# Kernel optimization log

Measured on AMD Instinct MI355X. Metric: run time of the kernel, lower is better.

## Reference

```python
import jax, jax.numpy as jnp
import numpy as np

PRUNING_THRESHOLD = 0.02


def setup_inputs() -> dict:
    key = jax.random.key(0)
    ks = jax.random.split(key, 9)
    B, T, D = 2, 2048, 512
    H, S = 8, 16
    hd = D // H
    x = jax.random.normal(ks[0], (B, T, D), dtype=jnp.float32)
    Wqkv = jax.random.normal(ks[1], (3 * D, D), dtype=jnp.float32) * 0.02
    Wout = jax.random.normal(ks[2], (D, D), dtype=jnp.float32) * 0.02
    splat_centers = jax.random.normal(ks[3], (H, S, hd), dtype=jnp.float32) * 0.3
    splat_deltas = jax.random.normal(ks[4], (H, S, hd), dtype=jnp.float32) * 0.05
    splat_log_scales = jax.random.normal(ks[5], (H, S), dtype=jnp.float32) * 0.2 + jnp.float32(np.log(0.5))
    splat_log_amplitudes = jax.random.normal(ks[6], (H, S), dtype=jnp.float32) * 0.1 - 0.5
    movement_scale = jnp.float32(0.08)
    temperature = jnp.float32(1.0)
    return {"x": x, "Wqkv": Wqkv, "Wout": Wout,
            "splat_centers": splat_centers, "splat_deltas": splat_deltas,
            "splat_log_scales": splat_log_scales, "splat_log_amplitudes": splat_log_amplitudes,
            "movement_scale": movement_scale, "temperature": temperature}


def reference(x, Wqkv, Wout, splat_centers, splat_deltas,
              splat_log_scales, splat_log_amplitudes, movement_scale, temperature):
    B, T, D = x.shape
    H, S, hd = splat_centers.shape
    # qkv projection (nn.Linear: y = x @ W.T), split into q,k,v per head
    qkv = (x @ Wqkv.T).reshape(B, T, 3, H, hd)
    q, k, v = qkv[:, :, 0], qkv[:, :, 1], qkv[:, :, 2]  # [B,T,H,hd]
    # effective centers with bounded movement (eval mode: no warmup)
    bounded_scale = jax.nn.sigmoid(movement_scale) * 0.2
    centers = splat_centers + splat_deltas * bounded_scale  # [H,S,hd]
    scales = jnp.clip(jnp.exp(splat_log_scales), 0.01, 2.0)  # [H,S]
    amplitudes = jnp.clip(jnp.exp(splat_log_amplitudes), 1e-06, 10.0)
    amplitudes = amplitudes * (amplitudes > PRUNING_THRESHOLD).astype(amplitudes.dtype)
    # squared distances from tokens to splat centers: [B,T,H,S]
    q_dists = jnp.sum((q[:, :, :, None, :] - centers[None, None]) ** 2, axis=-1)
    k_dists = jnp.sum((k[:, :, :, None, :] - centers[None, None]) ** 2, axis=-1)
    inv_var = 1.0 / (scales ** 2 + 1e-08)  # [H,S]
    q_w = jnp.exp(-0.5 * q_dists * inv_var)  # [B,T,H,S]
    k_w = jnp.exp(-0.5 * k_dists * inv_var)
    # per-head splat-weighted logits: [B,T(query i),T(key j),H]
    logits = jnp.einsum('bihs,bjhs,hs->bijh', q_w, k_w, amplitudes)
    temp = jnp.clip(temperature, 0.1, 10.0)
    # NOTE: original vectorized path softmaxes over dim=1 (query axis) -- faithful
    attn = jax.nn.softmax(logits / temp, axis=1)
    out = jnp.einsum('btjh,bjhd->bthd', attn, v).reshape(B, T, D)
    return out @ Wout.T
```

## Files before the change

kernel.cpp:

```cpp
#include <hip/hip_runtime.h>
#include <hip/hip_bf16.h>
#include <hip/hip_fp16.h>
#include <cstdint>
#include <cstddef>

#define T_SEQ 2048
#define NBATCH 2
#define DIMD 512
#define NH 8
#define NS 16
#define HD 64
#define NBH 16

using s16x8 = __attribute__((ext_vector_type(8))) short;
using f32x4 = __attribute__((ext_vector_type(4))) float;

static __device__ inline unsigned short f2bf(float f) {
  __hip_bfloat16 h = __float2bfloat16(f);
  return reinterpret_cast<unsigned short&>(h);
}
static __device__ inline unsigned short f2h(float f) {
  __half h = __float2half(f);
  return reinterpret_cast<unsigned short&>(h);
}
static __device__ inline float h2f(unsigned short u) {
  __half h = reinterpret_cast<__half&>(u);
  return __half2float(h);
}
static __device__ inline unsigned int pack2(float a, float b) {
  return (unsigned int)f2bf(a) | ((unsigned int)f2bf(b) << 16);
}
static __device__ inline void gload16(const void* g, void* l) {
  __builtin_amdgcn_global_load_lds((const __attribute__((address_space(1))) void*)g,
                                   (__attribute__((address_space(3))) void*)l, 16, 0, 0);
}
static __device__ inline int swz_id() {
  int nwg = gridDim.x * gridDim.y;
  int orig = blockIdx.y * gridDim.x + blockIdx.x;
  return (orig & 7) * (nwg >> 3) + (orig >> 3);
}

static const size_t OFF_VBUF = 0;
static const size_t OFF_AOUT = 2097152;
static const size_t OFF_XH   = 6291456;
static const size_t OFF_WQH  = 8388608;
static const size_t OFF_WOH  = 9175040;
static const size_t OFF_QABF = 9437184;
static const size_t OFF_KWBF = 9961472;
static const size_t OFF_SPART= 10485760;
static const size_t OFF_VPART= 10616832;
static const size_t OFF_CADJ = 10633216;
static const size_t OFF_IVAR = 10641408;
static const size_t OFF_AMPT = 10641536;

__global__ __launch_bounds__(256) void prep(
    const float* __restrict__ x, const float* __restrict__ Wqkv, const float* __restrict__ Wout,
    const float* __restrict__ centers, const float* __restrict__ deltas,
    const float* __restrict__ lsc, const float* __restrict__ lam,
    const float* __restrict__ ms, const float* __restrict__ tp,
    unsigned short* __restrict__ xh, unsigned short* __restrict__ wqh,
    unsigned short* __restrict__ woh,
    float* __restrict__ cadj, float* __restrict__ ivar, float* __restrict__ ampt) {
  int bid = blockIdx.x;
  int tid = threadIdx.x;
  if (bid == 3072) {
    float bscale = 0.2f / (1.0f + expf(-ms[0]));
    float tclip = fminf(fmaxf(tp[0], 0.1f), 10.0f);
    if (tid < NH * NS) {
      float sc = fminf(fmaxf(expf(lsc[tid]), 0.01f), 2.0f);
      ivar[tid] = 1.0f / (sc * sc + 1e-8f);
      float am = fminf(fmaxf(expf(lam[tid]), 1e-6f), 10.0f);
      am = (am > 0.02f) ? am : 0.0f;
      ampt[tid] = am / tclip;
    }
    for (int e = tid; e < NH * NS * HD; e += 256)
      cadj[e] = centers[e] + deltas[e] * bscale;
    return;
  }
  const float* src; unsigned short* dh; int i4;
  if (bid < 2048)      { src = x;    dh = xh;  i4 = bid * 256 + tid; }
  else if (bid < 2816) { src = Wqkv; dh = wqh; i4 = (bid - 2048) * 256 + tid; }
  else                 { src = Wout; dh = woh; i4 = (bid - 2816) * 256 + tid; }
  float4 v = *(const float4*)&src[(size_t)i4 * 4];
  ushort4 hh;
  hh.x = f2h(v.x); hh.y = f2h(v.y); hh.z = f2h(v.z); hh.w = f2h(v.w);
  *(ushort4*)&dh[(size_t)i4 * 4] = hh;
}

template<int BM, int BN>
__device__ __forceinline__ void gemm_core(
    const unsigned short* Ah, const unsigned short* Bh,
    int K, int m0, int n0,
    unsigned short* ash, unsigned short* bsh,
    f32x4 (&acc)[BM / 32][BN / 32]) {
  constexpr int WM = BM / 2, WN = BN / 2;
  constexpr int MF = WM / 16, NF = WN / 16;
  constexpr int NSA = BM / 8, NSB = BN / 8;
  constexpr int TSEG = NSA + NSB;
  int tid = threadIdx.x;
  int w = tid >> 6, l = tid & 63, lm = l & 15, lq = l >> 4;
  int wm = w >> 1, wn = w & 1;
  int r8 = l >> 3, c8 = l & 7;
  int ksl = (c8 ^ (r8 & 7)) << 3;
#pragma unroll
  for (int mi = 0; mi < MF; ++mi)
#pragma unroll
    for (int ni = 0; ni < NF; ++ni) acc[mi][ni] = (f32x4){0.f, 0.f, 0.f, 0.f};

  for (int k0 = 0; k0 < K; k0 += 64) {
    __syncthreads();
#pragma unroll
    for (int t = 0; t < TSEG / 4; ++t) {
      int s = w + t * 4;
      if (s < NSA) {
        gload16(&Ah[(size_t)(m0 + s * 8 + r8) * K + k0 + ksl], &ash[s * 512]);
      } else {
        int ss = s - NSA;
        gload16(&Bh[(size_t)(n0 + ss * 8 + r8) * K + k0 + ksl], &bsh[ss * 512]);
      }
    }
    __syncthreads();
#pragma unroll
    for (int kh = 0; kh < 2; ++kh) {
      s16x8 fah[MF], fbh[NF];
#pragma unroll
      for (int mi = 0; mi < MF; ++mi) {
        int rr = wm * WM + mi * 16 + lm;
        int off = rr * 64 + ((((kh << 2) | lq) ^ (rr & 7)) << 3);
        fah[mi] = *(const s16x8*)&ash[off];
      }
#pragma unroll
      for (int ni = 0; ni < NF; ++ni) {
        int cc = wn * WN + ni * 16 + lm;
        int off = cc * 64 + ((((kh << 2) | lq) ^ (cc & 7)) << 3);
        fbh[ni] = *(const s16x8*)&bsh[off];
      }
#pragma unroll
      for (int mi = 0; mi < MF; ++mi)
#pragma unroll
        for (int ni = 0; ni < NF; ++ni)
          acc[mi][ni] = __builtin_amdgcn_mfma_f32_16x16x32_f16(fah[mi], fbh[ni], acc[mi][ni], 0, 0, 0);
    }
  }
}

template<int BM, int BN>
__device__ __forceinline__ void write_c(
    float* C, int ldc, int m0, int n0, f32x4 (&acc)[BM / 32][BN / 32]) {
  constexpr int WM = BM / 2, WN = BN / 2;
  int tid = threadIdx.x;
  int w = tid >> 6, l = tid & 63, lm = l & 15, lq = l >> 4;
  int wm = w >> 1, wn = w & 1;
#pragma unroll
  for (int mi = 0; mi < BM / 32; ++mi)
#pragma unroll
    for (int ni = 0; ni < BN / 32; ++ni)
#pragma unroll
      for (int r = 0; r < 4; ++r) {
        int row = m0 + wm * WM + mi * 16 + lq * 4 + r;
        int col = n0 + wn * WN + ni * 16 + lm;
        C[(size_t)row * ldc + col] = acc[mi][ni][r];
      }
}

template<int BM, int BN>
__device__ __forceinline__ void write_ch(
    unsigned short* C, int ldc, int m0, int n0, f32x4 (&acc)[BM / 32][BN / 32]) {
  constexpr int WM = BM / 2, WN = BN / 2;
  int tid = threadIdx.x;
  int w = tid >> 6, l = tid & 63, lm = l & 15, lq = l >> 4;
  int wm = w >> 1, wn = w & 1;
#pragma unroll
  for (int mi = 0; mi < BM / 32; ++mi)
#pragma unroll
    for (int ni = 0; ni < BN / 32; ++ni)
#pragma unroll
      for (int r = 0; r < 4; ++r) {
        int row = m0 + wm * WM + mi * 16 + lq * 4 + r;
        int col = n0 + wn * WN + ni * 16 + lm;
        C[(size_t)row * ldc + col] = f2h(acc[mi][ni][r]);
      }
}

__global__ __launch_bounds__(256) void gemm_qkv(
    const unsigned short* __restrict__ xh, const unsigned short* __restrict__ wqh,
    const float* __restrict__ cadj, const float* __restrict__ ivar,
    const float* __restrict__ ampt, unsigned short* __restrict__ vbuf,
    unsigned short* __restrict__ qa_bf, unsigned short* __restrict__ kw_bf) {
  __shared__ __align__(16) char smem[39168];
  unsigned short* ash = (unsigned short*)smem;
  unsigned short* bsh = (unsigned short*)(smem + 16384);
  int sid = swz_id();
  int bx = sid % 24, by = sid / 24;
  int m0 = by * 128;
  int tid = threadIdx.x;
  f32x4 acc[4][2];
  if (bx >= 16) {
    gemm_core<128, 64>(xh, wqh + (size_t)(1024 + (bx - 16) * 64) * 512,
                       512, m0, 0, ash, bsh, acc);
    write_ch<128, 64>(vbuf, 512, m0, (bx - 16) * 64, acc);
    return;
  }
  bool isk = bx >= 8;
  int h = bx & 7;
  gemm_core<128, 64>(xh, wqh + (size_t)((isk ? 512 : 0) + h * 64) * 512,
                     512, m0, 0, ash, bsh, acc);
  __syncthreads();
  float* q_s = (float*)smem;
  float* c_s = (float*)(smem + 34816);
  {
    int w = tid >> 6, l = tid & 63, lm = l & 15, lq = l >> 4;
    int wm = w >> 1, wn = w & 1;
#pragma unroll
    for (int mi = 0; mi < 4; ++mi)
#pragma unroll
      for (int ni = 0; ni < 2; ++ni)
#pragma unroll
        for (int r = 0; r < 4; ++r)
          q_s[(wm * 64 + mi * 16 + lq * 4 + r) * 68 + wn * 32 + ni * 16 + lm] = acc[mi][ni][r];
    int cr = tid >> 4, d4 = tid & 15;
    *(float4*)&c_s[cr * 68 + d4 * 4] = *(const float4*)&cadj[(h * 16 + cr) * 64 + d4 * 4];
  }
  __syncthreads();
  int s = tid & 15, rbase = tid >> 4;
  float iv = ivar[h * 16 + s];
  float am = ampt[h * 16 + s];
  const float4* crow = (const float4*)&c_s[s * 68];
#pragma unroll
  for (int t = 0; t < 8; ++t) {
    int r = t * 16 + rbase;
    const float4* qrow = (const float4*)&q_s[r * 68];
    float d2 = 0.0f;
#pragma unroll
    for (int d4 = 0; d4 < 16; ++d4) {
      float4 qv = qrow[d4], cv = crow[d4];
      float e0 = qv.x - cv.x, e1 = qv.y - cv.y, e2 = qv.z - cv.z, e3 = qv.w - cv.w;
      d2 = fmaf(e0, e0, d2); d2 = fmaf(e1, e1, d2);
      d2 = fmaf(e2, e2, d2); d2 = fmaf(e3, e3, d2);
    }
    float val = __expf(-0.5f * d2 * iv);
    int row = m0 + r;
    int b = row >> 11, i = row & 2047;
    size_t base = ((size_t)(b * 8 + h) * T_SEQ + i) * 32;
    if (!isk) {
      qa_bf[base + s] = f2bf(val * am);
      qa_bf[base + 16 + s] = 0;
    } else {
      int xorv = (r >> 1) & 3;
      int slot = s >> 3, e = s & 7;
      kw_bf[base + (size_t)((slot ^ xorv) << 3) + e] = f2bf(val);
      kw_bf[base + (size_t)(((2 + slot) ^ xorv) << 3) + e] = 0;
    }
  }
}

__global__ __launch_bounds__(256) void gemm_out(
    const unsigned short* __restrict__ aout_h, const unsigned short* __restrict__ woh,
    float* __restrict__ out) {
  __shared__ __align__(16) unsigned short ash[64 * 64];
  __shared__ __align__(16) unsigned short bsh[64 * 64];
  int sid = swz_id();
  int bx = sid % 8, by = sid / 8;
  f32x4 acc[2][2];
  gemm_core<64, 64>(aout_h + (size_t)by * 64 * 512, woh + (size_t)bx * 64 * 512,
                    512, 0, 0, ash, bsh, acc);
  write_c<64, 64>(out, 512, by * 64, bx * 64, acc);
}

__global__ __launch_bounds__(256) void k3_colsum(
    const unsigned short* __restrict__ qa_bf, const unsigned short* __restrict__ kw_bf,
    float* __restrict__ spart) {
  int sid = swz_id();
  int jblk = sid & 15, yy = sid >> 4;
  int bh = yy >> 2, iq = yy & 3;
  int tid = threadIdx.x;
  int w = tid >> 6, l = tid & 63, lm = l & 15, lq = l >> 4;
  int jbase = (jblk << 7) + (w << 5);
  int sw = lq ^ ((lm >> 1) & 3);
  size_t base32 = (size_t)bh * T_SEQ * 32;
  s16x8 kwB0 = *(const s16x8*)&kw_bf[base32 + (size_t)(jbase + lm) * 32 + sw * 8];
  s16x8 kwB1 = *(const s16x8*)&kw_bf[base32 + (size_t)(jbase + 16 + lm) * 32 + sw * 8];
  const unsigned short* qp = qa_bf + base32 + ((size_t)(iq * 512) + lm) * 32 + lq * 8;
  float s0 = 0.0f, s1 = 0.0f;
  f32x4 z = (f32x4){0.f, 0.f, 0.f, 0.f};
#pragma unroll 4
  for (int it = 0; it < 512; it += 16) {
    s16x8 qaA = *(const s16x8*)(qp + (size_t)it * 32);
    f32x4 L0 = __builtin_amdgcn_mfma_f32_16x16x32_bf16(qaA, kwB0, z, 0, 0, 0);
    f32x4 L1 = __builtin_amdgcn_mfma_f32_16x16x32_bf16(qaA, kwB1, z, 0, 0, 0);
    s0 += (__expf(L0[0]) - 1.0f) + (__expf(L0[1]) - 1.0f)
        + (__expf(L0[2]) - 1.0f) + (__expf(L0[3]) - 1.0f);
    s1 += (__expf(L1[0]) - 1.0f) + (__expf(L1[1]) - 1.0f)
        + (__expf(L1[2]) - 1.0f) + (__expf(L1[3]) - 1.0f);
  }
  s0 += __shfl_xor(s0, 16); s0 += __shfl_xor(s0, 32);
  s1 += __shfl_xor(s1, 16); s1 += __shfl_xor(s1, 32);
  if (l < 16) {
    float* sp = spart + ((size_t)iq * NBH + bh) * T_SEQ;
    sp[jbase + lm] = s0;
    sp[jbase + 16 + lm] = s1;
  }
}

__global__ __launch_bounds__(256) void k3c_vt(
    const unsigned short* __restrict__ vbuf, const float* __restrict__ spart,
    unsigned short* __restrict__ vt, float* __restrict__ vpart) {
  int bh = blockIdx.y; int b = bh >> 3, h = bh & 7;
  int js = blockIdx.x << 7;
  int tid = threadIdx.x;
  __shared__ unsigned short t_s[64][136];
  __shared__ float red[16][64];
  int jg = tid >> 4, dq = tid & 15;
  const unsigned short* vb = vbuf + (size_t)b * T_SEQ * 512 + h * 64;
  const float* sp0 = spart + (size_t)bh * T_SEQ + js;
  const float* sp1 = spart + ((size_t)NBH + bh) * T_SEQ + js;
  const float* sp2 = spart + ((size_t)2 * NBH + bh) * T_SEQ + js;
  const float* sp3 = spart + ((size_t)3 * NBH + bh) * T_SEQ + js;
  float a0 = 0.f, a1 = 0.f, a2 = 0.f, a3 = 0.f;
#pragma unroll
  for (int p = 0; p < 8; ++p) {
    int j = p * 16 + jg;
    float s = 1.0f / (2048.0f + sp0[j] + sp1[j] + sp2[j] + sp3[j]);
    ushort4 vu = *(const ushort4*)&vb[(size_t)(js + j) * 512 + dq * 4];
    float v0 = h2f(vu.x) * s, v1 = h2f(vu.y) * s, v2 = h2f(vu.z) * s, v3 = h2f(vu.w) * s;
    t_s[dq * 4 + 0][j] = f2bf(v0);
    t_s[dq * 4 + 1][j] = f2bf(v1);
    t_s[dq * 4 + 2][j] = f2bf(v2);
    t_s[dq * 4 + 3][j] = f2bf(v3);
    a0 += v0; a1 += v1; a2 += v2; a3 += v3;
  }
  red[jg][dq * 4 + 0] = a0; red[jg][dq * 4 + 1] = a1;
  red[jg][dq * 4 + 2] = a2; red[jg][dq * 4 + 3] = a3;
  __syncthreads();
  if (tid < 64) {
    float t = 0.f;
#pragma unroll
    for (int g = 0; g < 16; ++g) t += red[g][tid];
    vpart[((size_t)blockIdx.x * NBH + bh) * 64 + tid] = t;
  }
#pragma unroll
  for (int p = 0; p < 4; ++p) {
    int idx = p * 256 + tid;
    int d = idx >> 4, seg = idx & 15;
    int4 val = *(const int4*)&t_s[d][seg * 8];
    int col = ((seg >> 3) << 6) + ((((seg & 7) ^ (d & 7))) << 3);
    *(int4*)&vt[(size_t)bh * 131072 + (size_t)d * 2048 + js + col] = val;
  }
}

__global__ __launch_bounds__(1024) void k4_attnout(
    const unsigned short* __restrict__ qa_bf, const unsigned short* __restrict__ kw_bf,
    const unsigned short* __restrict__ vt, const float* __restrict__ vpart,
    unsigned short* __restrict__ aout_h) {
  int sid = swz_id();
  int bh = sid >> 4; int b = bh >> 3, h = bh & 7;
  int i0 = (sid & 15) << 7;
  int tid = threadIdx.x;
  int w = tid >> 6, l = tid & 63, lm = l & 15, lq = l >> 4;
  int ig = w >> 2, jq = w & 3;
  __shared__ __align__(16) char smem[98304];
  unsigned short* kwS = (unsigned short*)smem;
  unsigned short* vtS = (unsigned short*)(smem + 32768);
  float* mrg = (float*)smem;
  const unsigned short* kwg = kw_bf + (size_t)bh * (T_SEQ * 32) + (size_t)jq * (512 * 32);
  const unsigned short* vtg = vt + (size_t)bh * 131072 + jq * 512;
  int p0 = ((lm >> 2) << 3) | (lm & 3);
  int sw0 = lq ^ ((lm >> 1) & 1);
  int sw1 = sw0 ^ 2;
  int swv = lm & 7;
  s16x8 qaB0 = *(const s16x8*)&qa_bf[((size_t)bh * T_SEQ + i0 + ig * 32 + lm) * 32 + lq * 8];
  s16x8 qaB1 = *(const s16x8*)&qa_bf[((size_t)bh * T_SEQ + i0 + ig * 32 + 16 + lm) * 32 + lq * 8];
  f32x4 acc[2][4];
#pragma unroll
  for (int ifr = 0; ifr < 2; ++ifr)
#pragma unroll
    for (int df = 0; df < 4; ++df) acc[ifr][df] = (f32x4){0.f, 0.f, 0.f, 0.f};
  f32x4 z = (f32x4){0.f, 0.f, 0.f, 0.f};

  auto stage = [&](int c, int bsel) {
#pragma unroll
    for (int t = 0; t < 2; ++t) {
      int li = ig * 2 + t;
      gload16(&vtg[(size_t)(li * 8 + (l >> 3)) * 2048 + c * 64 + (l & 7) * 8],
              &vtS[(jq * 2 + bsel) * 4096 + li * 512]);
    }
    gload16(&kwg[(size_t)(c * 64 + ig * 16 + (l >> 2)) * 32 + (l & 3) * 8],
            &kwS[(jq * 2 + bsel) * 2048 + ig * 512]);
  };

  stage(0, 0);
  __syncthreads();
  for (int c = 0; c < 8; ++c) {
    int bsel = c & 1;
    if (c < 7) stage(c + 1, bsel ^ 1);
    const unsigned short* kwb = &kwS[(jq * 2 + bsel) * 2048];
    const unsigned short* vtb = &vtS[(jq * 2 + bsel) * 4096];
#pragma unroll
    for (int s = 0; s < 2; ++s) {
      s16x8 ka0 = *(const s16x8*)&kwb[(s * 32 + p0) * 32 + sw0 * 8];
      s16x8 ka1 = *(const s16x8*)&kwb[(s * 32 + p0 + 4) * 32 + sw1 * 8];
      s16x8 vb0 = *(const s16x8*)&vtb[(size_t)(0 + lm) * 64 + (((4 * s + lq) ^ swv) << 3)];
      s16x8 vb1 = *(const s16x8*)&vtb[(size_t)(16 + lm) * 64 + (((4 * s + lq) ^ swv) << 3)];
      s16x8 vb2 = *(const s16x8*)&vtb[(size_t)(32 + lm) * 64 + (((4 * s + lq) ^ swv) << 3)];
      s16x8 vb3 = *(const s16x8*)&vtb[(size_t)(48 + lm) * 64 + (((4 * s + lq) ^ swv) << 3)];
#pragma unroll
      for (int ifr = 0; ifr < 2; ++ifr) {
        s16x8 qaB = ifr ? qaB1 : qaB0;
        f32x4 L0 = __builtin_amdgcn_mfma_f32_16x16x32_bf16(ka0, qaB, z, 0, 0, 0);
        f32x4 L1 = __builtin_amdgcn_mfma_f32_16x16x32_bf16(ka1, qaB, z, 0, 0, 0);
        union { unsigned int u4[4]; s16x8 v; } cvt;
        cvt.u4[0] = pack2(__expf(L0[0]) - 1.0f, __expf(L0[1]) - 1.0f);
        cvt.u4[1] = pack2(__expf(L0[2]) - 1.0f, __expf(L0[3]) - 1.0f);
        cvt.u4[2] = pack2(__expf(L1[0]) - 1.0f, __expf(L1[1]) - 1.0f);
        cvt.u4[3] = pack2(__expf(L1[2]) - 1.0f, __expf(L1[3]) - 1.0f);
        s16x8 pA = cvt.v;
        __builtin_amdgcn_s_setprio(1);
        acc[ifr][0] = __builtin_amdgcn_mfma_f32_16x16x32_bf16(pA, vb0, acc[ifr][0], 0, 0, 0);
        acc[ifr][1] = __builtin_amdgcn_mfma_f32_16x16x32_bf16(pA, vb1, acc[ifr][1], 0, 0, 0);
        acc[ifr][2] = __builtin_amdgcn_mfma_f32_16x16x32_bf16(pA, vb2, acc[ifr][2], 0, 0, 0);
        acc[ifr][3] = __builtin_amdgcn_mfma_f32_16x16x32_bf16(pA, vb3, acc[ifr][3], 0, 0, 0);
        __builtin_amdgcn_s_setprio(0);
      }
    }
    __syncthreads();
  }
  if (jq != 0) {
    int base = ((jq - 1) * 4 + ig) * 2;
#pragma unroll
    for (int ifr = 0; ifr < 2; ++ifr)
#pragma unroll
      for (int df = 0; df < 4; ++df)
#pragma unroll
        for (int r = 0; r < 4; ++r)
          mrg[(((base + ifr) * 4 + df) * 4 + r) * 64 + l] = acc[ifr][df][r];
  }
  __syncthreads();
  if (jq == 0) {
#pragma unroll
    for (int ifr = 0; ifr < 2; ++ifr)
#pragma unroll
      for (int df = 0; df < 4; ++df) {
        int d = df * 16 + lm;
        float vs = 0.0f;
#pragma unroll
        for (int js = 0; js < 16; ++js) vs += vpart[((size_t)js * NBH + bh) * 64 + d];
#pragma unroll
        for (int r = 0; r < 4; ++r) {
          int row = i0 + ig * 32 + ifr * 16 + lq * 4 + r;
          float o = acc[ifr][df][r] + vs;
#pragma unroll
          for (int jm = 0; jm < 3; ++jm)
            o += mrg[((((jm * 4 + ig) * 2 + ifr) * 4 + df) * 4 + r) * 64 + l];
          aout_h[((size_t)b * T_SEQ + row) * DIMD + h * 64 + d] = f2h(o);
        }
      }
  }
}

extern "C" void kernel_launch(void* const* d_in, const int* in_sizes, int n_in,
                              void* d_out, int out_size, void* d_ws, size_t ws_size,
                              hipStream_t stream) {
  const float* x    = (const float*)d_in[0];
  const float* Wqkv = (const float*)d_in[1];
  const float* Wout = (const float*)d_in[2];
  const float* ctr  = (const float*)d_in[3];
  const float* dlt  = (const float*)d_in[4];
  const float* lsc  = (const float*)d_in[5];
  const float* lam  = (const float*)d_in[6];
  const float* ms   = (const float*)d_in[7];
  const float* tp   = (const float*)d_in[8];
  float* ws = (float*)d_ws;
  unsigned short* vbuf   = (unsigned short*)(ws + OFF_VBUF);
  unsigned short* aout_h = (unsigned short*)(ws + OFF_AOUT);
  unsigned short* xh  = (unsigned short*)(ws + OFF_XH);
  unsigned short* wqh = (unsigned short*)(ws + OFF_WQH);
  unsigned short* woh = (unsigned short*)(ws + OFF_WOH);
  unsigned short* qa_bf = (unsigned short*)(ws + OFF_QABF);
  unsigned short* kw_bf = (unsigned short*)(ws + OFF_KWBF);
  float* spart = ws + OFF_SPART;
  float* vpart = ws + OFF_VPART;
  float* cadj  = ws + OFF_CADJ;
  float* ivar  = ws + OFF_IVAR;
  float* ampt  = ws + OFF_AMPT;
  unsigned short* vt = xh;
  float* out = (float*)d_out;

  prep<<<3073, 256, 0, stream>>>(x, Wqkv, Wout, ctr, dlt, lsc, lam, ms, tp,
                                 xh, wqh, woh, cadj, ivar, ampt);
  gemm_qkv<<<dim3(24, 32), 256, 0, stream>>>(xh, wqh, cadj, ivar, ampt,
                                             vbuf, qa_bf, kw_bf);
  k3_colsum<<<dim3(16, 64), 256, 0, stream>>>(qa_bf, kw_bf, spart);
  k3c_vt<<<dim3(16, 16), 256, 0, stream>>>(vbuf, spart, vt, vpart);
  k4_attnout<<<dim3(16, 16), 1024, 0, stream>>>(qa_bf, kw_bf, vt, vpart, aout_h);
  gemm_out<<<dim3(8, 64), 256, 0, stream>>>(aout_h, woh, out);
}
```

Baseline: 79.44 us.

## Fuse column-sum and V-transpose kernels and fold log2e into amplitudes

Merges the softmax column-sum kernel and the V scaling/transpose kernel into one 1024-thread kernel per (batch-head, key block). The partial column sums are reduced in shared memory instead of being written to and re-read from a global scratch buffer, which removes one launch and that round trip. The amplitude scale now includes log2(e), so exp2f replaces __expf in both the column-sum and attention kernels. The fused grid has only 256 large blocks, fewer than the old 1024-block column-sum grid, which may reduce latency hiding.

```diff
diff --git a/kernel.cpp b/kernel.cpp
--- a/kernel.cpp
+++ b/kernel.cpp
@@ -47,7 +47,6 @@
 static const size_t OFF_WOH  = 9175040;
 static const size_t OFF_QABF = 9437184;
 static const size_t OFF_KWBF = 9961472;
-static const size_t OFF_SPART= 10485760;
 static const size_t OFF_VPART= 10616832;
 static const size_t OFF_CADJ = 10633216;
 static const size_t OFF_IVAR = 10641408;
@@ -71,7 +70,7 @@
       ivar[tid] = 1.0f / (sc * sc + 1e-8f);
       float am = fminf(fmaxf(expf(lam[tid]), 1e-6f), 10.0f);
       am = (am > 0.02f) ? am : 0.0f;
-      ampt[tid] = am / tclip;
+      ampt[tid] = (am / tclip) * 1.44269504088896340736f;
     }
     for (int e = tid; e < NH * NS * HD; e += 256)
       cadj[e] = centers[e] + deltas[e] * bscale;
@@ -267,60 +266,71 @@
   write_c<64, 64>(out, 512, by * 64, bx * 64, acc);
 }
 
-__global__ __launch_bounds__(256) void k3_colsum(
+__global__ __launch_bounds__(1024) void k3_fused(
     const unsigned short* __restrict__ qa_bf, const unsigned short* __restrict__ kw_bf,
-    float* __restrict__ spart) {
+    const unsigned short* __restrict__ vbuf,
+    unsigned short* __restrict__ vt, float* __restrict__ vpart) {
   int sid = swz_id();
-  int jblk = sid & 15, yy = sid >> 4;
-  int bh = yy >> 2, iq = yy & 3;
+  int bh = sid >> 4; int b = bh >> 3, h = bh & 7;
+  int jblk = sid & 15;
+  int js = jblk << 7;
   int tid = threadIdx.x;
   int w = tid >> 6, l = tid & 63, lm = l & 15, lq = l >> 4;
-  int jbase = (jblk << 7) + (w << 5);
+  int iq = w >> 1, jh = w & 1;
+  __shared__ float red[8][128];
+  __shared__ float sinv_s[128];
+  __shared__ unsigned short t_s[64][136];
+  __shared__ float red2[64][64];
   int sw = lq ^ ((lm >> 1) & 3);
   size_t base32 = (size_t)bh * T_SEQ * 32;
+  int jbase = js + jh * 64;
   s16x8 kwB0 = *(const s16x8*)&kw_bf[base32 + (size_t)(jbase + lm) * 32 + sw * 8];
   s16x8 kwB1 = *(const s16x8*)&kw_bf[base32 + (size_t)(jbase + 16 + lm) * 32 + sw * 8];
-  const unsigned short* qp = qa_bf + base32 + ((size_t)(iq * 512) + lm) * 32 + lq * 8;
-  float s0 = 0.0f, s1 = 0.0f;
+  s16x8 kwB2 = *(const s16x8*)&kw_bf[base32 + (size_t)(jbase + 32 + lm) * 32 + sw * 8];
+  s16x8 kwB3 = *(const s16x8*)&kw_bf[base32 + (size_t)(jbase + 48 + lm) * 32 + sw * 8];
+  const unsigned short* qp = qa_bf + base32 + ((size_t)(iq * 256) + lm) * 32 + lq * 8;
+  float s0 = 0.f, s1 = 0.f, s2 = 0.f, s3 = 0.f;
   f32x4 z = (f32x4){0.f, 0.f, 0.f, 0.f};
 #pragma unroll 4
-  for (int it = 0; it < 512; it += 16) {
+  for (int it = 0; it < 256; it += 16) {
     s16x8 qaA = *(const s16x8*)(qp + (size_t)it * 32);
     f32x4 L0 = __builtin_amdgcn_mfma_f32_16x16x32_bf16(qaA, kwB0, z, 0, 0, 0);
     f32x4 L1 = __builtin_amdgcn_mfma_f32_16x16x32_bf16(qaA, kwB1, z, 0, 0, 0);
-    s0 += (__expf(L0[0]) - 1.0f) + (__expf(L0[1]) - 1.0f)
-        + (__expf(L0[2]) - 1.0f) + (__expf(L0[3]) - 1.0f);
-    s1 += (__expf(L1[0]) - 1.0f) + (__expf(L1[1]) - 1.0f)
-        + (__expf(L1[2]) - 1.0f) + (__expf(L1[3]) - 1.0f);
+    f32x4 L2 = __builtin_amdgcn_mfma_f32_16x16x32_bf16(qaA, kwB2, z, 0, 0, 0);
+    f32x4 L3 = __builtin_amdgcn_mfma_f32_16x16x32_bf16(qaA, kwB3, z, 0, 0, 0);
+    s0 += (exp2f(L0[0]) - 1.0f) + (exp2f(L0[1]) - 1.0f)
+        + (exp2f(L0[2]) - 1.0f) + (exp2f(L0[3]) - 1.0f);
+    s1 += (exp2f(L1[0]) - 1.0f) + (exp2f(L1[1]) - 1.0f)
+        + (exp2f(L1[2]) - 1.0f) + (exp2f(L1[3]) - 1.0f);
+    s2 += (exp2f(L2[0]) - 1.0f) + (exp2f(L2[1]) - 1.0f)
+        + (exp2f(L2[2]) - 1.0f) + (exp2f(L2[3]) - 1.0f);
+    s3 += (exp2f(L3[0]) - 1.0f) + (exp2f(L3[1]) - 1.0f)
+        + (exp2f(L3[2]) - 1.0f) + (exp2f(L3[3]) - 1.0f);
   }
   s0 += __shfl_xor(s0, 16); s0 += __shfl_xor(s0, 32);
   s1 += __shfl_xor(s1, 16); s1 += __shfl_xor(s1, 32);
+  s2 += __shfl_xor(s2, 16); s2 += __shfl_xor(s2, 32);
+  s3 += __shfl_xor(s3, 16); s3 += __shfl_xor(s3, 32);
   if (l < 16) {
-    float* sp = spart + ((size_t)iq * NBH + bh) * T_SEQ;
-    sp[jbase + lm] = s0;
-    sp[jbase + 16 + lm] = s1;
-  }
-}
-
-__global__ __launch_bounds__(256) void k3c_vt(
-    const unsigned short* __restrict__ vbuf, const float* __restrict__ spart,
-    unsigned short* __restrict__ vt, float* __restrict__ vpart) {
-  int bh = blockIdx.y; int b = bh >> 3, h = bh & 7;
-  int js = blockIdx.x << 7;
-  int tid = threadIdx.x;
-  __shared__ unsigned short t_s[64][136];
-  __shared__ float red[16][64];
+    red[iq][jh * 64 + lm] = s0;
+    red[iq][jh * 64 + 16 + lm] = s1;
+    red[iq][jh * 64 + 32 + lm] = s2;
+    red[iq][jh * 64 + 48 + lm] = s3;
+  }
+  __syncthreads();
+  if (tid < 128) {
+    float t = red[0][tid] + red[1][tid] + red[2][tid] + red[3][tid]
+            + red[4][tid] + red[5][tid] + red[6][tid] + red[7][tid];
+    sinv_s[tid] = 1.0f / (2048.0f + t);
+  }
+  __syncthreads();
   int jg = tid >> 4, dq = tid & 15;
   const unsigned short* vb = vbuf + (size_t)b * T_SEQ * 512 + h * 64;
-  const float* sp0 = spart + (size_t)bh * T_SEQ + js;
-  const float* sp1 = spart + ((size_t)NBH + bh) * T_SEQ + js;
-  const float* sp2 = spart + ((size_t)2 * NBH + bh) * T_SEQ + js;
-  const float* sp3 = spart + ((size_t)3 * NBH + bh) * T_SEQ + js;
   float a0 = 0.f, a1 = 0.f, a2 = 0.f, a3 = 0.f;
 #pragma unroll
-  for (int p = 0; p < 8; ++p) {
-    int j = p * 16 + jg;
-    float s = 1.0f / (2048.0f + sp0[j] + sp1[j] + sp2[j] + sp3[j]);
+  for (int p = 0; p < 2; ++p) {
+    int j = p * 64 + jg;
+    float s = sinv_s[j];
     ushort4 vu = *(const ushort4*)&vb[(size_t)(js + j) * 512 + dq * 4];
     float v0 = h2f(vu.x) * s, v1 = h2f(vu.y) * s, v2 = h2f(vu.z) * s, v3 = h2f(vu.w) * s;
     t_s[dq * 4 + 0][j] = f2bf(v0);
@@ -329,19 +339,17 @@
     t_s[dq * 4 + 3][j] = f2bf(v3);
     a0 += v0; a1 += v1; a2 += v2; a3 += v3;
   }
-  red[jg][dq * 4 + 0] = a0; red[jg][dq * 4 + 1] = a1;
-  red[jg][dq * 4 + 2] = a2; red[jg][dq * 4 + 3] = a3;
+  red2[jg][dq * 4 + 0] = a0; red2[jg][dq * 4 + 1] = a1;
+  red2[jg][dq * 4 + 2] = a2; red2[jg][dq * 4 + 3] = a3;
   __syncthreads();
   if (tid < 64) {
     float t = 0.f;
-#pragma unroll
-    for (int g = 0; g < 16; ++g) t += red[g][tid];
-    vpart[((size_t)blockIdx.x * NBH + bh) * 64 + tid] = t;
-  }
-#pragma unroll
-  for (int p = 0; p < 4; ++p) {
-    int idx = p * 256 + tid;
-    int d = idx >> 4, seg = idx & 15;
+#pragma unroll 8
+    for (int g = 0; g < 64; ++g) t += red2[g][tid];
+    vpart[((size_t)jblk * NBH + bh) * 64 + tid] = t;
+  }
+  {
+    int d = tid >> 4, seg = tid & 15;
     int4 val = *(const int4*)&t_s[d][seg * 8];
     int col = ((seg >> 3) << 6) + ((((seg & 7) ^ (d & 7))) << 3);
     *(int4*)&vt[(size_t)bh * 131072 + (size_t)d * 2048 + js + col] = val;
@@ -409,10 +417,10 @@
         f32x4 L0 = __builtin_amdgcn_mfma_f32_16x16x32_bf16(ka0, qaB, z, 0, 0, 0);
         f32x4 L1 = __builtin_amdgcn_mfma_f32_16x16x32_bf16(ka1, qaB, z, 0, 0, 0);
         union { unsigned int u4[4]; s16x8 v; } cvt;
-        cvt.u4[0] = pack2(__expf(L0[0]) - 1.0f, __expf(L0[1]) - 1.0f);
-        cvt.u4[1] = pack2(__expf(L0[2]) - 1.0f, __expf(L0[3]) - 1.0f);
-        cvt.u4[2] = pack2(__expf(L1[0]) - 1.0f, __expf(L1[1]) - 1.0f);
-        cvt.u4[3] = pack2(__expf(L1[2]) - 1.0f, __expf(L1[3]) - 1.0f);
+        cvt.u4[0] = pack2(exp2f(L0[0]) - 1.0f, exp2f(L0[1]) - 1.0f);
+        cvt.u4[1] = pack2(exp2f(L0[2]) - 1.0f, exp2f(L0[3]) - 1.0f);
+        cvt.u4[2] = pack2(exp2f(L1[0]) - 1.0f, exp2f(L1[1]) - 1.0f);
+        cvt.u4[3] = pack2(exp2f(L1[2]) - 1.0f, exp2f(L1[3]) - 1.0f);
         s16x8 pA = cvt.v;
         __builtin_amdgcn_s_setprio(1);
         acc[ifr][0] = __builtin_amdgcn_mfma_f32_16x16x32_bf16(pA, vb0, acc[ifr][0], 0, 0, 0);
@@ -477,7 +485,6 @@
   unsigned short* woh = (unsigned short*)(ws + OFF_WOH);
   unsigned short* qa_bf = (unsigned short*)(ws + OFF_QABF);
   unsigned short* kw_bf = (unsigned short*)(ws + OFF_KWBF);
-  float* spart = ws + OFF_SPART;
   float* vpart = ws + OFF_VPART;
   float* cadj  = ws + OFF_CADJ;
   float* ivar  = ws + OFF_IVAR;
@@ -489,8 +496,7 @@
                                  xh, wqh, woh, cadj, ivar, ampt);
   gemm_qkv<<<dim3(24, 32), 256, 0, stream>>>(xh, wqh, cadj, ivar, ampt,
                                              vbuf, qa_bf, kw_bf);
-  k3_colsum<<<dim3(16, 64), 256, 0, stream>>>(qa_bf, kw_bf, spart);
-  k3c_vt<<<dim3(16, 16), 256, 0, stream>>>(vbuf, spart, vt, vpart);
+  k3_fused<<<dim3(16, 16), 1024, 0, stream>>>(qa_bf, kw_bf, vbuf, vt, vpart);
   k4_attnout<<<dim3(16, 16), 1024, 0, stream>>>(qa_bf, kw_bf, vt, vpart, aout_h);
   gemm_out<<<dim3(8, 64), 256, 0, stream>>>(aout_h, woh, out);
 }
```

New measurement: 86.15 us. +8.4%, slower.
